# Kernel optimization log

Measured on AMD Instinct MI355X. Metric: run time of the kernel, lower is better.

The kernel has to match this reference:

```python
import jax, jax.numpy as jnp
import numpy as np

N, C, W = 64, 64, 4096
F, WW = 64, 9

def next_power2(n):
    return int(2 ** np.ceil(np.log2(n)))

def setup_inputs() -> dict:
    key = jax.random.key(0)
    k1, k2, k3 = jax.random.split(key, 3)
    x = jax.random.normal(k1, (N, C, W), dtype=jnp.float32)
    filt = jax.random.normal(k2, (F, C, WW), dtype=jnp.float32)
    bias = jax.random.normal(k3, (F,), dtype=jnp.float32)
    return {"x": x, "filt": filt, "bias": bias}

def reference(x, filt, bias):
    # FFT-based valid cross-correlation, no spectral compression
    # (preserve_energy_rate=None, index_back=None, out_size=None, padding=None).
    n_, c_, w_ = x.shape
    f_, _, ww_ = filt.shape
    out_W = w_ - ww_ + 1  # valid correlation output length
    fftsize = next_power2(w_ + ww_ - 1)
    xf = jnp.fft.rfft(x, n=fftsize)            # [N, C, K] complex64
    wf = jnp.fft.rfft(filt, n=fftsize)         # [F, C, K] complex64
    # correlation = ifft(Xf * conj(Wf)); sum over channels in freq domain
    of = jnp.einsum('nck,fck->nfk', xf, jnp.conj(wf))  # [N, F, K]
    out = jnp.fft.irfft(of, n=fftsize)[..., :out_W]    # [N, F, out_W] float32
    # original adds bias[f] once per channel iteration -> C * bias
    out = out + (c_ * bias)[None, :, None]
    return out
```

## Files before the change

### kernel.cpp

```cpp
#include <hip/hip_runtime.h>
#include <stdint.h>

#define N_   64
#define C_   64
#define W_   4096
#define F_   64
#define WW_  9
#define OW_  4088
#define WBLK 128
#define WROWS 136

typedef __bf16 bf16x8 __attribute__((ext_vector_type(8)));
typedef float  f32x4  __attribute__((ext_vector_type(4)));

__device__ __forceinline__ unsigned short f2bf(float f) {
    union { float f; uint32_t u; } v; v.f = f;
    uint32_t u = v.u;
    return (unsigned short)((u + 0x7FFFu + ((u >> 16) & 1u)) >> 16);
}

__global__ __launch_bounds__(256) void prep_filt_k(const float* __restrict__ filt,
                                                   unsigned short* __restrict__ filtB) {
    int id = blockIdx.x * 256 + threadIdx.x;
    if (id < WW_ * F_ * C_) {
        int j    = id & 7;
        int lane = (id >> 3) & 63;
        int u    = (id >> 9) & 1;
        int m    = (id >> 10) & 1;
        int f0h  = (id >> 11) & 1;
        int t    = id >> 12;
        int l15  = lane & 15, lg = lane >> 4;
        int f = f0h * 32 + u * 16 + l15;
        int c = m * 32 + lg * 8 + j;
        filtB[id] = f2bf(filt[(f * C_ + c) * WW_ + t]);
    }
}

__global__ __launch_bounds__(256, 8) void conv_k(const float* __restrict__ x,
                                                 const unsigned short* __restrict__ filtB,
                                                 const float* __restrict__ bias,
                                                 float* __restrict__ out) {
    __shared__ unsigned short xs[WROWS * 64];

    const int tid  = threadIdx.x;
    const int lane = tid & 63;
    const int wv   = tid >> 6;
    const int n    = blockIdx.y;
    const int w0   = blockIdx.x * WBLK;

    {
        const int c4 = (wv << 4) + (((tid >> 4) & 3) << 2);
        const int wq = (tid & 15) << 2;
        const int cg = c4 >> 3;
        const int cs = c4 & 7;
        const float* xb = x + ((size_t)(n * C_ + c4)) * W_ + w0;
        #pragma unroll
        for (int j = 0; j < 2; ++j) {
            const int wl = wq + j * 64;
            float4 r0 = *reinterpret_cast<const float4*>(xb + 0 * W_ + wl);
            float4 r1 = *reinterpret_cast<const float4*>(xb + 1 * W_ + wl);
            float4 r2 = *reinterpret_cast<const float4*>(xb + 2 * W_ + wl);
            float4 r3 = *reinterpret_cast<const float4*>(xb + 3 * W_ + wl);
            const float* p0 = &r0.x; const float* p1 = &r1.x;
            const float* p2 = &r2.x; const float* p3 = &r3.x;
            #pragma unroll
            for (int jj = 0; jj < 4; ++jj) {
                int w = wl + jj;
                ushort4 u;
                u.x = f2bf(p0[jj]); u.y = f2bf(p1[jj]);
                u.z = f2bf(p2[jj]); u.w = f2bf(p3[jj]);
                *reinterpret_cast<ushort4*>(&xs[w * 64 + ((cg ^ (w & 7)) << 3) + cs]) = u;
            }
        }
        if (tid < 32) {
            const int hc4 = (tid & 15) << 2;
            const int hwl = 128 + ((tid >> 4) << 2);
            const int hcg = hc4 >> 3;
            const int hcs = hc4 & 7;
            #pragma unroll
            for (int jj = 0; jj < 4; ++jj) {
                int w  = hwl + jj;
                int gw = w0 + w;
                ushort4 u;
                if (gw < W_) {
                    const float* hp = x + ((size_t)(n * C_ + hc4)) * W_ + gw;
                    u.x = f2bf(hp[0]);
                    u.y = f2bf(hp[(size_t)W_]);
                    u.z = f2bf(hp[(size_t)2 * W_]);
                    u.w = f2bf(hp[(size_t)3 * W_]);
                } else {
                    u.x = u.y = u.z = u.w = 0;
                }
                *reinterpret_cast<ushort4*>(&xs[w * 64 + ((hcg ^ (w & 7)) << 3) + hcs]) = u;
            }
        }
    }
    __syncthreads();

    const int f0h = wv & 1;
    const int whb = (wv >> 1) * 64;
    const int l15 = lane & 15;
    const int lg  = lane >> 4;

    const unsigned short* Bb = filtB + f0h * 2048 + lane * 8;
    const float bv0 = 64.0f * bias[f0h * 32 + l15];
    const float bv1 = 64.0f * bias[f0h * 32 + 16 + l15];

    f32x4 acc[4][2];
    #pragma unroll
    for (int s = 0; s < 4; ++s) {
        acc[s][0] = (f32x4){0.f, 0.f, 0.f, 0.f};
        acc[s][1] = (f32x4){0.f, 0.f, 0.f, 0.f};
    }

    #pragma unroll
    for (int t = 0; t < WW_; ++t) {
        #pragma unroll
        for (int m = 0; m < 2; ++m) {
            bf16x8 b0 = *reinterpret_cast<const bf16x8*>(Bb + t * 4096 + m * 1024);
            bf16x8 b1 = *reinterpret_cast<const bf16x8*>(Bb + t * 4096 + m * 1024 + 512);
            #pragma unroll
            for (int s = 0; s < 4; ++s) {
                int row   = whb + s * 16 + l15 + t;
                int chunk = ((m << 2) | lg) ^ (row & 7);
                bf16x8 a  = *reinterpret_cast<const bf16x8*>(&xs[row * 64 + chunk * 8]);
                acc[s][0] = __builtin_amdgcn_mfma_f32_16x16x32_bf16(a, b0, acc[s][0], 0, 0, 0);
                acc[s][1] = __builtin_amdgcn_mfma_f32_16x16x32_bf16(a, b1, acc[s][1], 0, 0, 0);
            }
        }
    }

    const int fb = f0h * 32 + l15;
    #pragma unroll
    for (int s = 0; s < 4; ++s) {
        int wg = w0 + whb + s * 16 + lg * 4;
        if (wg < OW_) {
            float4 o0, o1;
            o0.x = acc[s][0][0] + bv0; o0.y = acc[s][0][1] + bv0;
            o0.z = acc[s][0][2] + bv0; o0.w = acc[s][0][3] + bv0;
            o1.x = acc[s][1][0] + bv1; o1.y = acc[s][1][1] + bv1;
            o1.z = acc[s][1][2] + bv1; o1.w = acc[s][1][3] + bv1;
            *reinterpret_cast<float4*>(out + ((size_t)(n * F_ + fb) * OW_ + wg))      = o0;
            *reinterpret_cast<float4*>(out + ((size_t)(n * F_ + fb + 16) * OW_ + wg)) = o1;
        }
    }
}

extern "C" void kernel_launch(void* const* d_in, const int* in_sizes, int n_in,
                              void* d_out, int out_size, void* d_ws, size_t ws_size,
                              hipStream_t stream) {
    const float* x    = (const float*)d_in[0];
    const float* filt = (const float*)d_in[1];
    const float* bias = (const float*)d_in[2];
    float* out        = (float*)d_out;

    unsigned short* filtB = (unsigned short*)d_ws;

    prep_filt_k<<<(WW_ * F_ * C_ + 255) / 256, 256, 0, stream>>>(filt, filtB);

    dim3 grid(W_ / WBLK, N_);
    conv_k<<<grid, 256, 0, stream>>>(x, filtB, bias, out);
}
```

Before: 48.88 us.

## Use single-wave blocks computing a 64x64 output tile with 4x4 MFMA register blocking

Replaces 256-thread blocks of four waves with 64-thread single-wave blocks, each covering 64 output positions for all 64 filters, which lets the block drop __syncthreads. Each wave now loads 4 A and 4 B fragments per step and issues 16 MFMAs, giving more operand reuse per register load, and raises instruction priority around the MFMA cluster. The fp32-to-bf16 conversion is switched to the packed v_cvt_pk_bf16_f32 instruction. In exchange, the 8-row halo is reloaded for every 64-wide tile, and the larger accumulator array raises register pressure, which limits occupancy.

Measured after the change: 48.79 us. Within noise of the previous version (-0.2%).

```diff
diff --git a/kernel.cpp b/kernel.cpp
--- a/kernel.cpp
+++ b/kernel.cpp
@@ -7,8 +7,8 @@
 #define F_   64
 #define WW_  9
 #define OW_  4088
-#define WBLK 128
-#define WROWS 136
+#define WBLK 64
+#define WROWS 72
 
 typedef __bf16 bf16x8 __attribute__((ext_vector_type(8)));
 typedef float  f32x4  __attribute__((ext_vector_type(4)));
@@ -19,129 +19,138 @@
     return (unsigned short)((u + 0x7FFFu + ((u >> 16) & 1u)) >> 16);
 }
 
+__device__ __forceinline__ uint2 pk4(float a, float b, float c, float d) {
+    uint2 r;
+    asm volatile("v_cvt_pk_bf16_f32 %0, %1, %2" : "=v"(r.x) : "v"(a), "v"(b));
+    asm volatile("v_cvt_pk_bf16_f32 %0, %1, %2" : "=v"(r.y) : "v"(c), "v"(d));
+    return r;
+}
+
 __global__ __launch_bounds__(256) void prep_filt_k(const float* __restrict__ filt,
                                                    unsigned short* __restrict__ filtB) {
     int id = blockIdx.x * 256 + threadIdx.x;
     if (id < WW_ * F_ * C_) {
         int j    = id & 7;
         int lane = (id >> 3) & 63;
-        int u    = (id >> 9) & 1;
-        int m    = (id >> 10) & 1;
-        int f0h  = (id >> 11) & 1;
+        int uu   = (id >> 9) & 3;
+        int m    = (id >> 11) & 1;
         int t    = id >> 12;
         int l15  = lane & 15, lg = lane >> 4;
-        int f = f0h * 32 + u * 16 + l15;
+        int f = uu * 16 + l15;
         int c = m * 32 + lg * 8 + j;
         filtB[id] = f2bf(filt[(f * C_ + c) * WW_ + t]);
     }
 }
 
-__global__ __launch_bounds__(256, 8) void conv_k(const float* __restrict__ x,
-                                                 const unsigned short* __restrict__ filtB,
-                                                 const float* __restrict__ bias,
-                                                 float* __restrict__ out) {
+__global__ __launch_bounds__(64, 3) void conv_k(const float* __restrict__ x,
+                                                const unsigned short* __restrict__ filtB,
+                                                const float* __restrict__ bias,
+                                                float* __restrict__ out) {
     __shared__ unsigned short xs[WROWS * 64];
 
-    const int tid  = threadIdx.x;
-    const int lane = tid & 63;
-    const int wv   = tid >> 6;
+    const int lane = threadIdx.x;
     const int n    = blockIdx.y;
     const int w0   = blockIdx.x * WBLK;
+    const int l15  = lane & 15;
+    const int lg   = lane >> 4;
 
     {
-        const int c4 = (wv << 4) + (((tid >> 4) & 3) << 2);
-        const int wq = (tid & 15) << 2;
-        const int cg = c4 >> 3;
-        const int cs = c4 & 7;
-        const float* xb = x + ((size_t)(n * C_ + c4)) * W_ + w0;
+        const int wq = l15 << 2;
+        const int cs = (lg << 2) & 7;
+        const float* xb = x + ((size_t)(n * C_ + (lg << 2))) * W_ + w0 + wq;
         #pragma unroll
-        for (int j = 0; j < 2; ++j) {
-            const int wl = wq + j * 64;
-            float4 r0 = *reinterpret_cast<const float4*>(xb + 0 * W_ + wl);
-            float4 r1 = *reinterpret_cast<const float4*>(xb + 1 * W_ + wl);
-            float4 r2 = *reinterpret_cast<const float4*>(xb + 2 * W_ + wl);
-            float4 r3 = *reinterpret_cast<const float4*>(xb + 3 * W_ + wl);
+        for (int i = 0; i < 4; ++i) {
+            const float* xi = xb + (size_t)(i * 16) * W_;
+            float4 r0 = *reinterpret_cast<const float4*>(xi);
+            float4 r1 = *reinterpret_cast<const float4*>(xi + W_);
+            float4 r2 = *reinterpret_cast<const float4*>(xi + 2 * W_);
+            float4 r3 = *reinterpret_cast<const float4*>(xi + 3 * W_);
+            const int cg = (lg >> 1) + (i << 1);
             const float* p0 = &r0.x; const float* p1 = &r1.x;
             const float* p2 = &r2.x; const float* p3 = &r3.x;
             #pragma unroll
             for (int jj = 0; jj < 4; ++jj) {
-                int w = wl + jj;
-                ushort4 u;
-                u.x = f2bf(p0[jj]); u.y = f2bf(p1[jj]);
-                u.z = f2bf(p2[jj]); u.w = f2bf(p3[jj]);
-                *reinterpret_cast<ushort4*>(&xs[w * 64 + ((cg ^ (w & 7)) << 3) + cs]) = u;
+                int w = wq + jj;
+                uint2 u2 = pk4(p0[jj], p1[jj], p2[jj], p3[jj]);
+                *reinterpret_cast<uint2*>(&xs[w * 64 + ((cg ^ (w & 7)) << 3) + cs]) = u2;
             }
         }
-        if (tid < 32) {
-            const int hc4 = (tid & 15) << 2;
-            const int hwl = 128 + ((tid >> 4) << 2);
+        if (lane < 32) {
+            const int hc4 = (lane >> 1) << 2;
+            const int hw  = 64 + ((lane & 1) << 2);
             const int hcg = hc4 >> 3;
             const int hcs = hc4 & 7;
+            const float* hp = x + ((size_t)(n * C_ + hc4)) * W_ + w0 + hw;
             #pragma unroll
             for (int jj = 0; jj < 4; ++jj) {
-                int w  = hwl + jj;
+                int w  = hw + jj;
                 int gw = w0 + w;
-                ushort4 u;
+                float a0 = 0.f, a1 = 0.f, a2 = 0.f, a3 = 0.f;
                 if (gw < W_) {
-                    const float* hp = x + ((size_t)(n * C_ + hc4)) * W_ + gw;
-                    u.x = f2bf(hp[0]);
-                    u.y = f2bf(hp[(size_t)W_]);
-                    u.z = f2bf(hp[(size_t)2 * W_]);
-                    u.w = f2bf(hp[(size_t)3 * W_]);
-                } else {
-                    u.x = u.y = u.z = u.w = 0;
+                    a0 = hp[jj];
+                    a1 = hp[jj + (size_t)W_];
+                    a2 = hp[jj + (size_t)2 * W_];
+                    a3 = hp[jj + (size_t)3 * W_];
                 }
-                *reinterpret_cast<ushort4*>(&xs[w * 64 + ((hcg ^ (w & 7)) << 3) + hcs]) = u;
+                uint2 u2 = pk4(a0, a1, a2, a3);
+                *reinterpret_cast<uint2*>(&xs[w * 64 + ((hcg ^ (w & 7)) << 3) + hcs]) = u2;
             }
         }
     }
-    __syncthreads();
 
-    const int f0h = wv & 1;
-    const int whb = (wv >> 1) * 64;
-    const int l15 = lane & 15;
-    const int lg  = lane >> 4;
+    const unsigned short* Bb = filtB + lane * 8;
 
-    const unsigned short* Bb = filtB + f0h * 2048 + lane * 8;
-    const float bv0 = 64.0f * bias[f0h * 32 + l15];
-    const float bv1 = 64.0f * bias[f0h * 32 + 16 + l15];
+    float bv[4];
+    #pragma unroll
+    for (int uu = 0; uu < 4; ++uu)
+        bv[uu] = 64.0f * bias[uu * 16 + l15];
 
-    f32x4 acc[4][2];
+    f32x4 acc[4][4];
     #pragma unroll
-    for (int s = 0; s < 4; ++s) {
-        acc[s][0] = (f32x4){0.f, 0.f, 0.f, 0.f};
-        acc[s][1] = (f32x4){0.f, 0.f, 0.f, 0.f};
-    }
+    for (int s = 0; s < 4; ++s)
+        #pragma unroll
+        for (int uu = 0; uu < 4; ++uu)
+            acc[s][uu] = (f32x4){0.f, 0.f, 0.f, 0.f};
 
     #pragma unroll
     for (int t = 0; t < WW_; ++t) {
         #pragma unroll
         for (int m = 0; m < 2; ++m) {
-            bf16x8 b0 = *reinterpret_cast<const bf16x8*>(Bb + t * 4096 + m * 1024);
-            bf16x8 b1 = *reinterpret_cast<const bf16x8*>(Bb + t * 4096 + m * 1024 + 512);
+            bf16x8 a[4];
             #pragma unroll
             for (int s = 0; s < 4; ++s) {
-                int row   = whb + s * 16 + l15 + t;
+                int row   = s * 16 + l15 + t;
                 int chunk = ((m << 2) | lg) ^ (row & 7);
-                bf16x8 a  = *reinterpret_cast<const bf16x8*>(&xs[row * 64 + chunk * 8]);
-                acc[s][0] = __builtin_amdgcn_mfma_f32_16x16x32_bf16(a, b0, acc[s][0], 0, 0, 0);
-                acc[s][1] = __builtin_amdgcn_mfma_f32_16x16x32_bf16(a, b1, acc[s][1], 0, 0, 0);
+                a[s] = *reinterpret_cast<const bf16x8*>(&xs[row * 64 + chunk * 8]);
             }
+            bf16x8 b[4];
+            #pragma unroll
+            for (int uu = 0; uu < 4; ++uu)
+                b[uu] = *reinterpret_cast<const bf16x8*>(Bb + (((t * 2 + m) * 4 + uu) << 9));
+            __builtin_amdgcn_s_setprio(1);
+            #pragma unroll
+            for (int s = 0; s < 4; ++s)
+                #pragma unroll
+                for (int uu = 0; uu < 4; ++uu)
+                    acc[s][uu] = __builtin_amdgcn_mfma_f32_16x16x32_bf16(a[s], b[uu], acc[s][uu], 0, 0, 0);
+            __builtin_amdgcn_s_setprio(0);
         }
     }
 
-    const int fb = f0h * 32 + l15;
     #pragma unroll
-    for (int s = 0; s < 4; ++s) {
-        int wg = w0 + whb + s * 16 + lg * 4;
-        if (wg < OW_) {
-            float4 o0, o1;
-            o0.x = acc[s][0][0] + bv0; o0.y = acc[s][0][1] + bv0;
-            o0.z = acc[s][0][2] + bv0; o0.w = acc[s][0][3] + bv0;
-            o1.x = acc[s][1][0] + bv1; o1.y = acc[s][1][1] + bv1;
-            o1.z = acc[s][1][2] + bv1; o1.w = acc[s][1][3] + bv1;
-            *reinterpret_cast<float4*>(out + ((size_t)(n * F_ + fb) * OW_ + wg))      = o0;
-            *reinterpret_cast<float4*>(out + ((size_t)(n * F_ + fb + 16) * OW_ + wg)) = o1;
+    for (int uu = 0; uu < 4; ++uu) {
+        const int f = uu * 16 + l15;
+        #pragma unroll
+        for (int s = 0; s < 4; ++s) {
+            int wg = w0 + s * 16 + lg * 4;
+            if (wg < OW_) {
+                float4 o;
+                o.x = acc[s][uu][0] + bv[uu];
+                o.y = acc[s][uu][1] + bv[uu];
+                o.z = acc[s][uu][2] + bv[uu];
+                o.w = acc[s][uu][3] + bv[uu];
+                *reinterpret_cast<float4*>(out + ((size_t)(n * F_ + f) * OW_ + wg)) = o;
+            }
         }
     }
 }
@@ -159,5 +168,5 @@
     prep_filt_k<<<(WW_ * F_ * C_ + 255) / 256, 256, 0, stream>>>(filt, filtB);
 
     dim3 grid(W_ / WBLK, N_);
-    conv_k<<<grid, 256, 0, stream>>>(x, filtB, bias, out);
+    conv_k<<<grid, 64, 0, stream>>>(x, filtB, bias, out);
 }
```
